# Performance work log

Hardware: AMD Instinct MI355X
Metric: run time of the kernel (lower is better)

The kernel has to match this reference:

```python
import jax, jax.numpy as jnp
import numpy as np

TIME_SEG_LEN = 5
PRED_STEPS = 1
B, N, D = 4, 4096, 4
F1, F2 = 32, 64  # cnn filters; F2 must equal GCSConv/Dense width 64


def _conv1d_time(x, Wc1, bc1, Wc2, bc2):
    # x: [B, N, T, D] -> per-node temporal CNN collapsing T=5 -> 1 -> [B, N, F2]
    b, n, t, d = x.shape
    xr = x.reshape(b * n, t, d)
    dn = ('NWC', 'WIO', 'NWC')
    h = jax.lax.conv_general_dilated(xr, Wc1, (1,), 'VALID', dimension_numbers=dn) + bc1
    h = jax.nn.relu(h)
    h = jax.lax.conv_general_dilated(h, Wc2, (1,), 'VALID', dimension_numbers=dn) + bc2
    return h.reshape(b, n, -1)  # [B, N, F2]


def setup_inputs() -> dict:
    key = jax.random.key(0)
    ks = jax.random.split(key, 12)
    time_segs = jax.random.normal(ks[0], (B, TIME_SEG_LEN, N, D), dtype=jnp.float32)
    edges = jax.random.randint(ks[1], (N, N), 0, 2, dtype=jnp.int32)
    s = lambda *sh: 1.0 / np.sqrt(sh[-2] if len(sh) > 1 else sh[0])
    return {
        'time_segs': time_segs,
        'edges': edges,
        'Wc1': jax.random.normal(ks[2], (3, D, F1), dtype=jnp.float32) * 0.3,
        'bc1': jnp.zeros((F1,), jnp.float32),
        'Wc2': jax.random.normal(ks[3], (3, F1, F2), dtype=jnp.float32) * 0.1,
        'bc2': jnp.zeros((F2,), jnp.float32),
        'Wg1': jax.random.normal(ks[4], (F2, 64), dtype=jnp.float32) * 0.125,
        'bg': jnp.zeros((64,), jnp.float32),
        'Wd': jax.random.normal(ks[5], (F2 + 64, 64), dtype=jnp.float32) * 0.09,
        'bd': jnp.zeros((64,), jnp.float32),
        'Wo': jax.random.normal(ks[6], (64, D), dtype=jnp.float32) * 0.125,
        'bo': jnp.zeros((D,), jnp.float32),
    }


def reference(time_segs, edges, Wc1, bc1, Wc2, bc2, Wg1, bg, Wd, bd, Wo, bo):
    A = edges.astype(jnp.float32)
    n = A.shape[0]
    deg = jnp.sum(A, axis=-1, keepdims=True)              # row degree
    A_norm = A / jnp.where(deg > 0, deg, 1.0)             # D^-1 A (symmetric=False)
    A_nd = A_norm * (1.0 - jnp.eye(n, dtype=A.dtype))     # self-edge masking of X row j == zeroing diag
    col_deg = jnp.sum(A, axis=0)                          # e = np.sum(edges, axis=0)
    alive = (col_deg != 0).astype(time_segs.dtype)[None, :, None]  # zero-degree nodes -> zeros branch

    ext = jnp.transpose(time_segs, (0, 2, 1, 3))          # [B, N, T, D]
    for i in range(PRED_STEPS):
        seg = ext[:, :, i:, :]                            # [B, N, 5, D]
        cond = _conv1d_time(seg, Wc1, bc1, Wc2, bc2)      # [B, N, F2]
        # Vectorized per-node masked GCSConv: row j of tanh(A X_j W1 + X_j W2 + b)
        # with X_j = X zeroed at node j. Skip term vanishes at row j.
        agg = jnp.einsum('jk,bkf->bjf', A_nd, cond)       # [B, N, F2]
        G = jnp.tanh(agg @ Wg1 + bg) * alive              # [B, N, 64]
        h = jax.nn.relu(jnp.concatenate([cond, G], axis=-1) @ Wd + bd)
        nxt = seg[:, :, -1, :] + jnp.tanh(h @ Wo + bo)    # residual update [B, N, D]
        ext = jnp.concatenate([ext, nxt[:, :, None, :]], axis=2)
    out = jnp.transpose(ext, (0, 2, 1, 3))                # [B, T+P, N, D]
    return out[:, TIME_SEG_LEN:, :, :]                    # [B, pred_steps, N, D]
```

## Files before the change

### kernel.cpp

```cpp
#include <hip/hip_runtime.h>
#include <math.h>

typedef unsigned short ushort_t;
typedef unsigned int uint_t;
typedef unsigned long long u64_t;
typedef __attribute__((ext_vector_type(8))) __bf16 bf16x8;
typedef __attribute__((ext_vector_type(4))) float f32x4;

#define NN 4096
#define TT 5
#define F1 32
#define F2 64

__device__ __forceinline__ ushort_t f2bf(float x) {
    union { float f; uint_t u; } v; v.f = x;
    uint_t r = (v.u + 0x7FFFu + ((v.u >> 16) & 1u)) >> 16;
    return (ushort_t)r;
}
__device__ __forceinline__ uint_t pk2(float a, float b) {
    return (uint_t)f2bf(a) | ((uint_t)f2bf(b) << 16);
}
__device__ __forceinline__ float tanh_fast(float x) {
    const float xc = fminf(fmaxf(x, -10.f), 10.f);
    const float e = __expf(2.f * xc);
    return (e - 1.f) * __builtin_amdgcn_rcpf(e + 1.f);
}

__global__ __launch_bounds__(256) void k0_prep(
    const float* __restrict__ Wc2, const float* __restrict__ Wg1, const float* __restrict__ Wd,
    ushort_t* __restrict__ Wc2T_ws, ushort_t* __restrict__ WgT_ws, ushort_t* __restrict__ WdT_ws,
    int* __restrict__ degI, uint_t* __restrict__ colbits)
{
    const int blk = blockIdx.x, t = threadIdx.x;
    if (blk == 0) {
        const uint4 z = make_uint4(0, 0, 0, 0);
        for (int i = t; i < 1024; i += 256) ((uint4*)degI)[i] = z;
        if (t < 32) ((uint4*)colbits)[t] = z;
    } else if (blk == 1) {
        for (int i = t; i < 6144; i += 256) {
            const int e = i >> 6, f = i & 63;
            Wc2T_ws[f * 96 + e] = f2bf(Wc2[i]);
        }
    } else if (blk == 2) {
        for (int i = t; i < 4096; i += 256) {
            const int in = i >> 6, o = i & 63;
            WgT_ws[o * 64 + in] = f2bf(Wg1[i]);
        }
    } else {
        for (int i = t; i < 8192; i += 256) {
            const int in = i >> 6, o = i & 63;
            WdT_ws[o * 128 + in] = f2bf(Wd[i]);
        }
    }
}

#define H1S 104
#define CBS 80
__global__ __launch_bounds__(256) void k1_cond(
    const float* __restrict__ ts, const float* __restrict__ Wc1, const float* __restrict__ bc1,
    const ushort_t* __restrict__ Wc2T_ws, const float* __restrict__ bc2,
    ushort_t* __restrict__ condT, ushort_t* __restrict__ condB)
{
    const int b = blockIdx.y;
    const int j0 = blockIdx.x * 64;
    const int t = threadIdx.x;

    __shared__ float sWc1[384];
    __shared__ float sbc1[F1];
    __shared__ float sbc2[F2];
    __shared__ ushort_t sWc2T[64 * H1S];
    __shared__ ushort_t h1B[64 * H1S];
    __shared__ ushort_t scb[64 * CBS];

    for (int i = t; i < 384; i += 256) sWc1[i] = Wc1[i];
    if (t < F1) sbc1[t] = bc1[t];
    if (t < F2) sbc2[t] = bc2[t];
    for (int i = t; i < 768; i += 256) {
        const int f = i / 12, c = i - f * 12;
        *(uint4*)&sWc2T[f * H1S + c * 8] = *(const uint4*)(Wc2T_ws + f * 96 + c * 8);
    }
    __syncthreads();

    {
        const int n = t & 63, f10 = (t >> 6) * 8;
        const int j = j0 + n;
        float4 x[5];
        #pragma unroll
        for (int tt = 0; tt < 5; ++tt)
            x[tt] = *(const float4*)(ts + ((((size_t)b * TT + tt) << 12) + j) * 4);
        #pragma unroll
        for (int tt0 = 0; tt0 < 3; ++tt0) {
            #pragma unroll
            for (int ff = 0; ff < 8; ++ff) {
                const int f1 = f10 + ff;
                float a = sbc1[f1];
                #pragma unroll
                for (int dt = 0; dt < 3; ++dt) {
                    const float4 xx = x[tt0 + dt];
                    a += xx.x * sWc1[(dt * 4 + 0) * F1 + f1];
                    a += xx.y * sWc1[(dt * 4 + 1) * F1 + f1];
                    a += xx.z * sWc1[(dt * 4 + 2) * F1 + f1];
                    a += xx.w * sWc1[(dt * 4 + 3) * F1 + f1];
                }
                h1B[n * H1S + tt0 * 32 + f1] = f2bf(fmaxf(a, 0.f));
            }
        }
    }
    __syncthreads();

    {
        const int w = t >> 6, l = t & 63;
        const int m0 = w * 16, kseg = (l >> 4) * 8;
        f32x4 acc[4] = {};
        #pragma unroll
        for (int ks = 0; ks < 3; ++ks) {
            const bf16x8 av = *(const bf16x8*)&h1B[(m0 + (l & 15)) * H1S + ks * 32 + kseg];
            #pragma unroll
            for (int ct = 0; ct < 4; ++ct) {
                const bf16x8 bv = *(const bf16x8*)&sWc2T[(ct * 16 + (l & 15)) * H1S + ks * 32 + kseg];
                acc[ct] = __builtin_amdgcn_mfma_f32_16x16x32_bf16(av, bv, acc[ct], 0, 0, 0);
            }
        }
        #pragma unroll
        for (int ct = 0; ct < 4; ++ct)
            #pragma unroll
            for (int i = 0; i < 4; ++i) {
                const int row = m0 + (l >> 4) * 4 + i;
                const int col = ct * 16 + (l & 15);
                scb[col * CBS + row] = f2bf(acc[ct][i] + sbc2[col]);
            }
    }
    __syncthreads();
    {
        const int f2 = t >> 2, seg = t & 3;
        ushort_t* dst = condT + (((size_t)b * 64 + f2) << 12) + j0 + seg * 16;
        *(uint4*)dst = *(const uint4*)&scb[f2 * CBS + seg * 16];
        *(uint4*)(dst + 8) = *(const uint4*)&scb[f2 * CBS + seg * 16 + 8];
    }
    {
        const int r = t >> 2, q = t & 3;
        uint_t u[8];
        #pragma unroll
        for (int k = 0; k < 8; ++k)
            u[k] = (uint_t)scb[(q * 16 + 2 * k) * CBS + r] |
                   ((uint_t)scb[(q * 16 + 2 * k + 1) * CBS + r] << 16);
        ushort_t* dstB = condB + ((((size_t)b << 12) + j0 + r) << 6) + q * 16;
        *(uint4*)dstB = make_uint4(u[0], u[1], u[2], u[3]);
        *(uint4*)(dstB + 8) = make_uint4(u[4], u[5], u[6], u[7]);
    }
}

__global__ __launch_bounds__(1024, 8) void k3_gemm(
    const int* __restrict__ edges, const ushort_t* __restrict__ condT,
    float* __restrict__ agg0, float* __restrict__ agg1,
    float* __restrict__ agg2, float* __restrict__ agg3,
    int* __restrict__ degI, uint_t* __restrict__ colbits,
    unsigned char* __restrict__ diagB)
{
    const int t = threadIdx.x;
    const int stripe = blockIdx.x >> 2, ks4 = blockIdx.x & 3;
    const int j0 = stripe * 32, kb = ks4 * 1024;

    __shared__ __align__(16) ushort_t abuf[8][4096];
    __shared__ uint_t colsh[32];
    __shared__ int sdeg[32];

    const int rl = t & 15, wq = (t >> 4) & 31, rh = t >> 9;
    const int row = j0 + rh * 16 + rl;
    const int* ep = edges + (size_t)row * NN + kb + wq * 32;
    int4 v[8];
    #pragma unroll
    for (int c = 0; c < 8; ++c) v[c] = *(const int4*)(ep + c * 4);
    if (t < 32) { colsh[t] = 0; sdeg[t] = 0; }
    uint_t bw = 0;
    #pragma unroll
    for (int c = 0; c < 8; ++c) {
        const uint_t nib = (v[c].x != 0 ? 1u : 0u) | (v[c].y != 0 ? 2u : 0u) |
                           (v[c].z != 0 ? 4u : 0u) | (v[c].w != 0 ? 8u : 0u);
        bw |= nib << (c * 4);
    }
    {
        ushort_t* dst = &abuf[wq >> 2][rh * 2048 + (wq & 3) * 512];
        #pragma unroll
        for (int o = 0; o < 4; ++o) {
            const uint_t oct = bw >> (o * 8);
            uint4 wv;
            wv.x = ((oct & 1u)   ? 0x3F80u : 0u) | ((oct & 2u)   ? 0x3F800000u : 0u);
            wv.y = ((oct & 4u)   ? 0x3F80u : 0u) | ((oct & 8u)   ? 0x3F800000u : 0u);
            wv.z = ((oct & 16u)  ? 0x3F80u : 0u) | ((oct & 32u)  ? 0x3F800000u : 0u);
            wv.w = ((oct & 64u)  ? 0x3F80u : 0u) | ((oct & 128u) ? 0x3F800000u : 0u);
            *(uint4*)(dst + o * 128 + ((rl * 8) ^ (o << 4))) = wv;
        }
    }
    if (((row - kb) >> 5) == wq)
        diagB[row] = (unsigned char)((bw >> ((row - kb) & 31)) & 1u);
    int s = __popc(bw);
    s += __shfl_down(s, 16);
    s += __shfl_down(s, 32);
    __syncthreads();
    if ((t & 63) < 16) atomicAdd(&sdeg[rh * 16 + rl], s);
    atomicOr(&colsh[wq], bw);

    const int w = t >> 6, l = t & 63;
    const int aoff = (l * 8) ^ ((l >> 4) << 4);
    const ushort_t* bp = condT + (size_t)(w * 16 + (l & 15)) * NN + kb + (l >> 4) * 8;

    f32x4 acc0 = {0.f, 0.f, 0.f, 0.f};
    f32x4 acc1 = {0.f, 0.f, 0.f, 0.f};

    #pragma unroll
    for (int ch = 0; ch < 8; ++ch) {
        const ushort_t* ab = &abuf[ch][0];
        const ushort_t* bpi = bp + ch * 128;
        #pragma unroll
        for (int ks = 0; ks < 4; ++ks) {
            const bf16x8 bfv = *(const bf16x8*)(bpi + ks * 32);
            const bf16x8 a0 = *(const bf16x8*)(ab + ks * 512 + aoff);
            const bf16x8 a1 = *(const bf16x8*)(ab + 2048 + ks * 512 + aoff);
            acc0 = __builtin_amdgcn_mfma_f32_16x16x32_bf16(a0, bfv, acc0, 0, 0, 0);
            acc1 = __builtin_amdgcn_mfma_f32_16x16x32_bf16(a1, bfv, acc1, 0, 0, 0);
        }
    }

    {
        float* aggS = (ks4 == 0) ? agg0 : (ks4 == 1) ? agg1 : (ks4 == 2) ? agg2 : agg3;
        const int col = w * 16 + (l & 15);
        float* dst = aggS + ((size_t)(col >> 6) * NN << 6) + (col & 63);
        #pragma unroll
        for (int i = 0; i < 4; ++i) {
            const int ja = j0 + (l >> 4) * 4 + i;
            dst[(size_t)ja << 6] = acc0[i];
            dst[(size_t)(ja + 16) << 6] = acc1[i];
        }
    }
    __syncthreads();
    if (t < 32) {
        atomicOr(&colbits[(kb >> 5) + t], colsh[t]);
        atomicAdd(&degI[j0 + t], sdeg[t]);
    }
}

#define WGS 88
#define WDS 136
#define HS  69
__global__ __launch_bounds__(256) void k4_mlp(
    const float* __restrict__ ts, const ushort_t* __restrict__ condB,
    const float* __restrict__ agg0, const float* __restrict__ agg1,
    const float* __restrict__ agg2, const float* __restrict__ agg3,
    const int* __restrict__ degI, const uint_t* __restrict__ colbits,
    const unsigned char* __restrict__ diagB,
    const ushort_t* __restrict__ WgT_ws, const float* __restrict__ bg,
    const ushort_t* __restrict__ WdT_ws, const float* __restrict__ bd,
    const float* __restrict__ Wo, const float* __restrict__ bo,
    float* __restrict__ out)
{
    const int b = blockIdx.y;
    const int j0 = blockIdx.x * 64;
    const int t = threadIdx.x;

    __shared__ ushort_t sWg1T[64 * WGS];
    __shared__ ushort_t sWdT[64 * WDS];
    __shared__ ushort_t aggB[64 * WGS];
    __shared__ ushort_t catB[64 * WDS];
    __shared__ float sH[64 * HS];
    __shared__ float sWo[256];
    __shared__ float sbg[64], sbd[64], sbo[4], sAlive[64];

    for (int i = t; i < 512; i += 256)
        *(uint4*)&sWg1T[(i >> 3) * WGS + (i & 7) * 8] = ((const uint4*)WgT_ws)[i];
    for (int i = t; i < 1024; i += 256)
        *(uint4*)&sWdT[(i >> 4) * WDS + (i & 15) * 8] = ((const uint4*)WdT_ws)[i];
    if (t < 256) sWo[t] = Wo[t];
    if (t < 64) { sbg[t] = bg[t]; sbd[t] = bd[t]; }
    if (t < 4) sbo[t] = bo[t];
    if (t < 64) {
        const int j = j0 + t;
        sAlive[t] = (float)((colbits[j >> 5] >> (j & 31)) & 1u);
    }
    {
        const int r = t >> 2, fs = t & 3;
        const int j = j0 + r;
        const float dv = (float)degI[j];
        const float inv = 1.f / (dv > 0.f ? dv : 1.f);
        const float dgf = (float)diagB[j];
        const size_t base = (((size_t)b << 12) + j) << 6;
        const uint4 c0 = *(const uint4*)(condB + base + fs * 16);
        const uint4 c1 = *(const uint4*)(condB + base + fs * 16 + 8);
        *(uint4*)&catB[r * WDS + fs * 16] = c0;
        *(uint4*)&catB[r * WDS + fs * 16 + 8] = c1;
        #pragma unroll
        for (int q = 0; q < 4; ++q) {
            uint_t wlo, whi;
            if (q == 0)      { wlo = c0.x; whi = c0.y; }
            else if (q == 1) { wlo = c0.z; whi = c0.w; }
            else if (q == 2) { wlo = c1.x; whi = c1.y; }
            else             { wlo = c1.z; whi = c1.w; }
            const int f = fs * 16 + q * 4;
            const float4 a0 = *(const float4*)(agg0 + base + f);
            const float4 a1 = *(const float4*)(agg1 + base + f);
            const float4 a2 = *(const float4*)(agg2 + base + f);
            const float4 a3 = *(const float4*)(agg3 + base + f);
            const float cv0 = __uint_as_float(wlo << 16);
            const float cv1 = __uint_as_float(wlo & 0xFFFF0000u);
            const float cv2 = __uint_as_float(whi << 16);
            const float cv3 = __uint_as_float(whi & 0xFFFF0000u);
            const float n0 = (a0.x + a1.x + a2.x + a3.x - dgf * cv0) * inv;
            const float n1 = (a0.y + a1.y + a2.y + a3.y - dgf * cv1) * inv;
            const float n2 = (a0.z + a1.z + a2.z + a3.z - dgf * cv2) * inv;
            const float n3 = (a0.w + a1.w + a2.w + a3.w - dgf * cv3) * inv;
            *(uint2*)&aggB[r * WGS + f] = make_uint2(pk2(n0, n1), pk2(n2, n3));
        }
    }
    __syncthreads();

    const int w = t >> 6, l = t & 63;
    const int m0 = w * 16, kseg = (l >> 4) * 8;

    {
        f32x4 acc[4] = {};
        #pragma unroll
        for (int ks = 0; ks < 2; ++ks) {
            const bf16x8 av = *(const bf16x8*)&aggB[(m0 + (l & 15)) * WGS + ks * 32 + kseg];
            #pragma unroll
            for (int ct = 0; ct < 4; ++ct) {
                const bf16x8 bv = *(const bf16x8*)&sWg1T[(ct * 16 + (l & 15)) * WGS + ks * 32 + kseg];
                acc[ct] = __builtin_amdgcn_mfma_f32_16x16x32_bf16(av, bv, acc[ct], 0, 0, 0);
            }
        }
        #pragma unroll
        for (int ct = 0; ct < 4; ++ct)
            #pragma unroll
            for (int i = 0; i < 4; ++i) {
                const int row = m0 + (l >> 4) * 4 + i;
                const int col = ct * 16 + (l & 15);
                const float g = tanh_fast(acc[ct][i] + sbg[col]) * sAlive[row];
                catB[row * WDS + 64 + col] = f2bf(g);
            }
    }
    __syncthreads();
    {
        f32x4 acc[4] = {};
        #pragma unroll
        for (int ks = 0; ks < 4; ++ks) {
            const bf16x8 av = *(const bf16x8*)&catB[(m0 + (l & 15)) * WDS + ks * 32 + kseg];
            #pragma unroll
            for (int ct = 0; ct < 4; ++ct) {
                const bf16x8 bv = *(const bf16x8*)&sWdT[(ct * 16 + (l & 15)) * WDS + ks * 32 + kseg];
                acc[ct] = __builtin_amdgcn_mfma_f32_16x16x32_bf16(av, bv, acc[ct], 0, 0, 0);
            }
        }
        #pragma unroll
        for (int ct = 0; ct < 4; ++ct)
            #pragma unroll
            for (int i = 0; i < 4; ++i) {
                const int row = m0 + (l >> 4) * 4 + i;
                const int col = ct * 16 + (l & 15);
                sH[row * HS + col] = fmaxf(acc[ct][i] + sbd[col], 0.f);
            }
    }
    __syncthreads();
    {
        const int r = t >> 2, d = t & 3;
        const int j = j0 + r;
        float s = sbo[d];
        #pragma unroll 8
        for (int f = 0; f < 64; ++f) s += sH[r * HS + f] * sWo[f * 4 + d];
        const float segl = ts[((((size_t)b * TT + 4) << 12) + j) * 4 + d];
        out[((((size_t)b << 12) + j) << 2) + d] = segl + tanh_fast(s);
    }
}

extern "C" void kernel_launch(void* const* d_in, const int* in_sizes, int n_in,
                              void* d_out, int out_size, void* d_ws, size_t ws_size,
                              hipStream_t stream)
{
    (void)in_sizes; (void)n_in; (void)out_size; (void)ws_size;
    const float* ts    = (const float*)d_in[0];
    const int*   edges = (const int*)d_in[1];
    const float* Wc1   = (const float*)d_in[2];
    const float* bc1   = (const float*)d_in[3];
    const float* Wc2   = (const float*)d_in[4];
    const float* bc2   = (const float*)d_in[5];
    const float* Wg1   = (const float*)d_in[6];
    const float* bg    = (const float*)d_in[7];
    const float* Wd    = (const float*)d_in[8];
    const float* bd    = (const float*)d_in[9];
    const float* Wo    = (const float*)d_in[10];
    const float* bo    = (const float*)d_in[11];
    float* out = (float*)d_out;

    char* ws = (char*)d_ws;
    ushort_t* condT   = (ushort_t*)(ws);
    ushort_t* condB   = (ushort_t*)(ws + (size_t)(2 << 20));
    float*    agg0    = (float*)(ws + (size_t)(4 << 20));
    float*    agg1    = (float*)(ws + (size_t)(8 << 20));
    float*    agg2    = (float*)(ws + (size_t)(12 << 20));
    float*    agg3    = (float*)(ws + (size_t)(16 << 20));
    int*      degI    = (int*)(ws + (size_t)(20 << 20));
    uint_t*   colbits = (uint_t*)(ws + (size_t)(20 << 20) + 16384);
    unsigned char* diagB = (unsigned char*)(ws + (size_t)(20 << 20) + 16896);
    ushort_t* WgT_ws  = (ushort_t*)(ws + (size_t)(20 << 20) + 20992);
    ushort_t* WdT_ws  = (ushort_t*)(ws + (size_t)(20 << 20) + 29184);
    ushort_t* Wc2T_ws = (ushort_t*)(ws + (size_t)(20 << 20) + 45568);

    k0_prep<<<4, 256, 0, stream>>>(Wc2, Wg1, Wd, Wc2T_ws, WgT_ws, WdT_ws, degI, colbits);
    k1_cond<<<dim3(64, 4), 256, 0, stream>>>(ts, Wc1, bc1, Wc2T_ws, bc2, condT, condB);
    k3_gemm<<<512, 1024, 0, stream>>>(edges, condT, agg0, agg1, agg2, agg3,
                                      degI, colbits, diagB);
    k4_mlp<<<dim3(64, 4), 256, 0, stream>>>(ts, condB, agg0, agg1, agg2, agg3,
                                            degI, colbits, diagB,
                                            WgT_ws, bg, WdT_ws, bd, Wo, bo, out);
}
```

Before: 174.2 us.

## Split edge bit-packing and degree computation into a separate kernel before GEMM

Adds a k2_bits kernel that reads the int32 adjacency matrix once, packs it into a bitmask in workspace, and computes row degrees, column-alive bits and diagonal flags without atomics on degI. The GEMM kernel then reads compact packed bits instead of 64 MB of int32 edges and drops its shared-memory reductions and global atomics. This adds a kernel launch and a bits write plus read round-trip, but both kernels keep the same total edge traffic while the GEMM becomes lighter.

```diff
diff --git a/kernel.cpp b/kernel.cpp
--- a/kernel.cpp
+++ b/kernel.cpp
@@ -29,13 +29,11 @@
 __global__ __launch_bounds__(256) void k0_prep(
     const float* __restrict__ Wc2, const float* __restrict__ Wg1, const float* __restrict__ Wd,
     ushort_t* __restrict__ Wc2T_ws, ushort_t* __restrict__ WgT_ws, ushort_t* __restrict__ WdT_ws,
-    int* __restrict__ degI, uint_t* __restrict__ colbits)
+    uint_t* __restrict__ colbits)
 {
     const int blk = blockIdx.x, t = threadIdx.x;
     if (blk == 0) {
-        const uint4 z = make_uint4(0, 0, 0, 0);
-        for (int i = t; i < 1024; i += 256) ((uint4*)degI)[i] = z;
-        if (t < 32) ((uint4*)colbits)[t] = z;
+        if (t < 32) ((uint4*)colbits)[t] = make_uint4(0, 0, 0, 0);
     } else if (blk == 1) {
         for (int i = t; i < 6144; i += 256) {
             const int e = i >> 6, f = i & 63;
@@ -52,6 +50,52 @@
             WdT_ws[o * 128 + in] = f2bf(Wd[i]);
         }
     }
+}
+
+__global__ __launch_bounds__(1024, 4) void k2_bits(
+    const int4* __restrict__ edges4, uint_t* __restrict__ bits,
+    int* __restrict__ degI, uint_t* __restrict__ colbits, unsigned char* __restrict__ diagB)
+{
+    const int t = threadIdx.x;
+    const int bid = blockIdx.x;
+    __shared__ int sdeg[16][8];
+
+    int4 v[8];
+    #pragma unroll
+    for (int s = 0; s < 8; ++s)
+        v[s] = edges4[(size_t)s * 524288 + (size_t)bid * 1024 + (size_t)t];
+
+    const int w = t >> 6, l = t & 63;
+    const int nsh = (t & 7) * 4;
+    uint_t creg = 0;
+    #pragma unroll
+    for (int s = 0; s < 8; ++s) {
+        const int row = s * 512 + bid;
+        const uint_t nib = (v[s].x != 0 ? 1u : 0u) | (v[s].y != 0 ? 2u : 0u) |
+                           (v[s].z != 0 ? 4u : 0u) | (v[s].w != 0 ? 8u : 0u);
+        uint_t part = nib << nsh;
+        part |= __shfl_xor(part, 1);
+        part |= __shfl_xor(part, 2);
+        part |= __shfl_xor(part, 4);
+        if ((t & 7) == 0) {
+            bits[(size_t)row * 128 + (size_t)(t >> 3)] = part;
+            creg |= part;
+            if ((t >> 3) == (row >> 5))
+                diagB[row] = (unsigned char)((part >> (row & 31)) & 1u);
+        }
+        int p = __popc(nib);
+        #pragma unroll
+        for (int off = 32; off >= 1; off >>= 1) p += __shfl_down(p, off);
+        if (l == 0) sdeg[w][s] = p;
+    }
+    __syncthreads();
+    if (t < 8) {
+        int s2 = 0;
+        #pragma unroll
+        for (int w2 = 0; w2 < 16; ++w2) s2 += sdeg[w2][t];
+        degI[t * 512 + bid] = s2;
+    }
+    if ((t & 7) == 0) atomicOr(&colbits[t >> 3], creg);
 }
 
 #define H1S 104
@@ -151,34 +195,18 @@
 }
 
 __global__ __launch_bounds__(1024, 8) void k3_gemm(
-    const int* __restrict__ edges, const ushort_t* __restrict__ condT,
+    const uint_t* __restrict__ bits, const ushort_t* __restrict__ condT,
     float* __restrict__ agg0, float* __restrict__ agg1,
-    float* __restrict__ agg2, float* __restrict__ agg3,
-    int* __restrict__ degI, uint_t* __restrict__ colbits,
-    unsigned char* __restrict__ diagB)
+    float* __restrict__ agg2, float* __restrict__ agg3)
 {
     const int t = threadIdx.x;
     const int stripe = blockIdx.x >> 2, ks4 = blockIdx.x & 3;
     const int j0 = stripe * 32, kb = ks4 * 1024;
 
     __shared__ __align__(16) ushort_t abuf[8][4096];
-    __shared__ uint_t colsh[32];
-    __shared__ int sdeg[32];
 
     const int rl = t & 15, wq = (t >> 4) & 31, rh = t >> 9;
-    const int row = j0 + rh * 16 + rl;
-    const int* ep = edges + (size_t)row * NN + kb + wq * 32;
-    int4 v[8];
-    #pragma unroll
-    for (int c = 0; c < 8; ++c) v[c] = *(const int4*)(ep + c * 4);
-    if (t < 32) { colsh[t] = 0; sdeg[t] = 0; }
-    uint_t bw = 0;
-    #pragma unroll
-    for (int c = 0; c < 8; ++c) {
-        const uint_t nib = (v[c].x != 0 ? 1u : 0u) | (v[c].y != 0 ? 2u : 0u) |
-                           (v[c].z != 0 ? 4u : 0u) | (v[c].w != 0 ? 8u : 0u);
-        bw |= nib << (c * 4);
-    }
+    const uint_t bw = bits[(size_t)(j0 + rh * 16 + rl) * 128 + (size_t)(kb >> 5) + (size_t)wq];
     {
         ushort_t* dst = &abuf[wq >> 2][rh * 2048 + (wq & 3) * 512];
         #pragma unroll
@@ -192,14 +220,7 @@
             *(uint4*)(dst + o * 128 + ((rl * 8) ^ (o << 4))) = wv;
         }
     }
-    if (((row - kb) >> 5) == wq)
-        diagB[row] = (unsigned char)((bw >> ((row - kb) & 31)) & 1u);
-    int s = __popc(bw);
-    s += __shfl_down(s, 16);
-    s += __shfl_down(s, 32);
-    __syncthreads();
-    if ((t & 63) < 16) atomicAdd(&sdeg[rh * 16 + rl], s);
-    atomicOr(&colsh[wq], bw);
+    __syncthreads();
 
     const int w = t >> 6, l = t & 63;
     const int aoff = (l * 8) ^ ((l >> 4) << 4);
@@ -232,11 +253,6 @@
             dst[(size_t)ja << 6] = acc0[i];
             dst[(size_t)(ja + 16) << 6] = acc1[i];
         }
-    }
-    __syncthreads();
-    if (t < 32) {
-        atomicOr(&colbits[(kb >> 5) + t], colsh[t]);
-        atomicAdd(&degI[j0 + t], sdeg[t]);
     }
 }
 
@@ -402,11 +418,12 @@
     ushort_t* WgT_ws  = (ushort_t*)(ws + (size_t)(20 << 20) + 20992);
     ushort_t* WdT_ws  = (ushort_t*)(ws + (size_t)(20 << 20) + 29184);
     ushort_t* Wc2T_ws = (ushort_t*)(ws + (size_t)(20 << 20) + 45568);
-
-    k0_prep<<<4, 256, 0, stream>>>(Wc2, Wg1, Wd, Wc2T_ws, WgT_ws, WdT_ws, degI, colbits);
+    uint_t*   bits    = (uint_t*)(ws + (size_t)(21 << 20));
+
+    k0_prep<<<4, 256, 0, stream>>>(Wc2, Wg1, Wd, Wc2T_ws, WgT_ws, WdT_ws, colbits);
+    k2_bits<<<512, 1024, 0, stream>>>((const int4*)edges, bits, degI, colbits, diagB);
     k1_cond<<<dim3(64, 4), 256, 0, stream>>>(ts, Wc1, bc1, Wc2T_ws, bc2, condT, condB);
-    k3_gemm<<<512, 1024, 0, stream>>>(edges, condT, agg0, agg1, agg2, agg3,
-                                      degI, colbits, diagB);
+    k3_gemm<<<512, 1024, 0, stream>>>(bits, condT, agg0, agg1, agg2, agg3);
     k4_mlp<<<dim3(64, 4), 256, 0, stream>>>(ts, condB, agg0, agg1, agg2, agg3,
                                             degI, colbits, diagB,
                                             WgT_ws, bg, WdT_ws, bd, Wo, bo, out);
```

New measurement: 189.7 us. 8.9% more time.

## Split edge bit-packing into separate kernel and fold weight prep into consumers

Applied to the files above, without the earlier changes.

A new k2_bits kernel reads the int32 adjacency once, packs it into a 2 MB bitmask, and computes row degrees with plain stores plus column-alive bits and diagonal flags. The GEMM kernel then reads the compact bits instead of the 64 MB edge matrix and drops its shared-memory atomics and tail reductions. The weight-transpose prep kernel is removed: k1 and k4 now convert and transpose weights from fp32 directly into shared memory, and a memset replaces the colbits zeroing. This adds a launch and a bitmask round trip through memory, and repeats the weight conversion in every block.

```diff
diff --git a/kernel.cpp b/kernel.cpp
--- a/kernel.cpp
+++ b/kernel.cpp
@@ -26,39 +26,53 @@
     return (e - 1.f) * __builtin_amdgcn_rcpf(e + 1.f);
 }
 
-__global__ __launch_bounds__(256) void k0_prep(
-    const float* __restrict__ Wc2, const float* __restrict__ Wg1, const float* __restrict__ Wd,
-    ushort_t* __restrict__ Wc2T_ws, ushort_t* __restrict__ WgT_ws, ushort_t* __restrict__ WdT_ws,
-    int* __restrict__ degI, uint_t* __restrict__ colbits)
+__global__ __launch_bounds__(1024, 8) void k2_bits(
+    const int4* __restrict__ edges4, uint_t* __restrict__ bits,
+    int* __restrict__ degI, uint_t* __restrict__ colbits, unsigned char* __restrict__ diagB)
 {
-    const int blk = blockIdx.x, t = threadIdx.x;
-    if (blk == 0) {
-        const uint4 z = make_uint4(0, 0, 0, 0);
-        for (int i = t; i < 1024; i += 256) ((uint4*)degI)[i] = z;
-        if (t < 32) ((uint4*)colbits)[t] = z;
-    } else if (blk == 1) {
-        for (int i = t; i < 6144; i += 256) {
-            const int e = i >> 6, f = i & 63;
-            Wc2T_ws[f * 96 + e] = f2bf(Wc2[i]);
-        }
-    } else if (blk == 2) {
-        for (int i = t; i < 4096; i += 256) {
-            const int in = i >> 6, o = i & 63;
-            WgT_ws[o * 64 + in] = f2bf(Wg1[i]);
-        }
-    } else {
-        for (int i = t; i < 8192; i += 256) {
-            const int in = i >> 6, o = i & 63;
-            WdT_ws[o * 128 + in] = f2bf(Wd[i]);
-        }
-    }
+    const int t = threadIdx.x;
+    const int bid = blockIdx.x;
+    const uint_t W = (uint_t)bid * 1024u + (uint_t)t;
+    __shared__ uint_t colsh[128];
+    __shared__ int sdeg[16];
+
+    const int4* ep = edges4 + (size_t)W * 8;
+    int4 v[8];
+    #pragma unroll
+    for (int c = 0; c < 8; ++c) v[c] = ep[c];
+
+    if (t < 128) colsh[t] = 0;
+
+    uint_t bw = 0;
+    #pragma unroll
+    for (int c = 0; c < 8; ++c) {
+        const uint_t nib = (v[c].x != 0 ? 1u : 0u) | (v[c].y != 0 ? 2u : 0u) |
+                           (v[c].z != 0 ? 4u : 0u) | (v[c].w != 0 ? 8u : 0u);
+        bw |= nib << (c * 4);
+    }
+    bits[W] = bw;
+
+    const int row = (int)(W >> 7);
+    if ((t & 127) == (row >> 5))
+        diagB[row] = (unsigned char)((bw >> (row & 31)) & 1u);
+
+    int s = __popc(bw);
+    #pragma unroll
+    for (int off = 32; off >= 1; off >>= 1) s += __shfl_down(s, off);
+    const int w = t >> 6, l = t & 63;
+    if (l == 0) sdeg[w] = s;
+    __syncthreads();
+    atomicOr(&colsh[t & 127], bw);
+    __syncthreads();
+    if (t < 128) atomicOr(&colbits[t], colsh[t]);
+    if (t < 8) degI[bid * 8 + t] = sdeg[2 * t] + sdeg[2 * t + 1];
 }
 
 #define H1S 104
 #define CBS 80
 __global__ __launch_bounds__(256) void k1_cond(
     const float* __restrict__ ts, const float* __restrict__ Wc1, const float* __restrict__ bc1,
-    const ushort_t* __restrict__ Wc2T_ws, const float* __restrict__ bc2,
+    const float* __restrict__ Wc2, const float* __restrict__ bc2,
     ushort_t* __restrict__ condT, ushort_t* __restrict__ condB)
 {
     const int b = blockIdx.y;
@@ -75,9 +89,9 @@
     for (int i = t; i < 384; i += 256) sWc1[i] = Wc1[i];
     if (t < F1) sbc1[t] = bc1[t];
     if (t < F2) sbc2[t] = bc2[t];
-    for (int i = t; i < 768; i += 256) {
-        const int f = i / 12, c = i - f * 12;
-        *(uint4*)&sWc2T[f * H1S + c * 8] = *(const uint4*)(Wc2T_ws + f * 96 + c * 8);
+    for (int i = t; i < 96 * 64; i += 256) {
+        const int e = i >> 6, f = i & 63;
+        sWc2T[f * H1S + e] = f2bf(Wc2[i]);
     }
     __syncthreads();
 
@@ -151,34 +165,18 @@
 }
 
 __global__ __launch_bounds__(1024, 8) void k3_gemm(
-    const int* __restrict__ edges, const ushort_t* __restrict__ condT,
+    const uint_t* __restrict__ bits, const ushort_t* __restrict__ condT,
     float* __restrict__ agg0, float* __restrict__ agg1,
-    float* __restrict__ agg2, float* __restrict__ agg3,
-    int* __restrict__ degI, uint_t* __restrict__ colbits,
-    unsigned char* __restrict__ diagB)
+    float* __restrict__ agg2, float* __restrict__ agg3)
 {
     const int t = threadIdx.x;
     const int stripe = blockIdx.x >> 2, ks4 = blockIdx.x & 3;
     const int j0 = stripe * 32, kb = ks4 * 1024;
 
     __shared__ __align__(16) ushort_t abuf[8][4096];
-    __shared__ uint_t colsh[32];
-    __shared__ int sdeg[32];
 
     const int rl = t & 15, wq = (t >> 4) & 31, rh = t >> 9;
-    const int row = j0 + rh * 16 + rl;
-    const int* ep = edges + (size_t)row * NN + kb + wq * 32;
-    int4 v[8];
-    #pragma unroll
-    for (int c = 0; c < 8; ++c) v[c] = *(const int4*)(ep + c * 4);
-    if (t < 32) { colsh[t] = 0; sdeg[t] = 0; }
-    uint_t bw = 0;
-    #pragma unroll
-    for (int c = 0; c < 8; ++c) {
-        const uint_t nib = (v[c].x != 0 ? 1u : 0u) | (v[c].y != 0 ? 2u : 0u) |
-                           (v[c].z != 0 ? 4u : 0u) | (v[c].w != 0 ? 8u : 0u);
-        bw |= nib << (c * 4);
-    }
+    const uint_t bw = bits[(size_t)(j0 + rh * 16 + rl) * 128 + (size_t)(kb >> 5) + (size_t)wq];
     {
         ushort_t* dst = &abuf[wq >> 2][rh * 2048 + (wq & 3) * 512];
         #pragma unroll
@@ -192,14 +190,7 @@
             *(uint4*)(dst + o * 128 + ((rl * 8) ^ (o << 4))) = wv;
         }
     }
-    if (((row - kb) >> 5) == wq)
-        diagB[row] = (unsigned char)((bw >> ((row - kb) & 31)) & 1u);
-    int s = __popc(bw);
-    s += __shfl_down(s, 16);
-    s += __shfl_down(s, 32);
-    __syncthreads();
-    if ((t & 63) < 16) atomicAdd(&sdeg[rh * 16 + rl], s);
-    atomicOr(&colsh[wq], bw);
+    __syncthreads();
 
     const int w = t >> 6, l = t & 63;
     const int aoff = (l * 8) ^ ((l >> 4) << 4);
@@ -232,11 +223,6 @@
             dst[(size_t)ja << 6] = acc0[i];
             dst[(size_t)(ja + 16) << 6] = acc1[i];
         }
-    }
-    __syncthreads();
-    if (t < 32) {
-        atomicOr(&colbits[(kb >> 5) + t], colsh[t]);
-        atomicAdd(&degI[j0 + t], sdeg[t]);
     }
 }
 
@@ -249,8 +235,8 @@
     const float* __restrict__ agg2, const float* __restrict__ agg3,
     const int* __restrict__ degI, const uint_t* __restrict__ colbits,
     const unsigned char* __restrict__ diagB,
-    const ushort_t* __restrict__ WgT_ws, const float* __restrict__ bg,
-    const ushort_t* __restrict__ WdT_ws, const float* __restrict__ bd,
+    const float* __restrict__ Wg1, const float* __restrict__ bg,
+    const float* __restrict__ Wd, const float* __restrict__ bd,
     const float* __restrict__ Wo, const float* __restrict__ bo,
     float* __restrict__ out)
 {
@@ -266,10 +252,14 @@
     __shared__ float sWo[256];
     __shared__ float sbg[64], sbd[64], sbo[4], sAlive[64];
 
-    for (int i = t; i < 512; i += 256)
-        *(uint4*)&sWg1T[(i >> 3) * WGS + (i & 7) * 8] = ((const uint4*)WgT_ws)[i];
-    for (int i = t; i < 1024; i += 256)
-        *(uint4*)&sWdT[(i >> 4) * WDS + (i & 15) * 8] = ((const uint4*)WdT_ws)[i];
+    for (int i = t; i < 4096; i += 256) {
+        const int in = i >> 6, o = i & 63;
+        sWg1T[o * WGS + in] = f2bf(Wg1[i]);
+    }
+    for (int i = t; i < 8192; i += 256) {
+        const int in = i >> 6, o = i & 63;
+        sWdT[o * WDS + in] = f2bf(Wd[i]);
+    }
     if (t < 256) sWo[t] = Wo[t];
     if (t < 64) { sbg[t] = bg[t]; sbd[t] = bd[t]; }
     if (t < 4) sbo[t] = bo[t];
@@ -399,15 +389,13 @@
     int*      degI    = (int*)(ws + (size_t)(20 << 20));
     uint_t*   colbits = (uint_t*)(ws + (size_t)(20 << 20) + 16384);
     unsigned char* diagB = (unsigned char*)(ws + (size_t)(20 << 20) + 16896);
-    ushort_t* WgT_ws  = (ushort_t*)(ws + (size_t)(20 << 20) + 20992);
-    ushort_t* WdT_ws  = (ushort_t*)(ws + (size_t)(20 << 20) + 29184);
-    ushort_t* Wc2T_ws = (ushort_t*)(ws + (size_t)(20 << 20) + 45568);
-
-    k0_prep<<<4, 256, 0, stream>>>(Wc2, Wg1, Wd, Wc2T_ws, WgT_ws, WdT_ws, degI, colbits);
-    k1_cond<<<dim3(64, 4), 256, 0, stream>>>(ts, Wc1, bc1, Wc2T_ws, bc2, condT, condB);
-    k3_gemm<<<512, 1024, 0, stream>>>(edges, condT, agg0, agg1, agg2, agg3,
-                                      degI, colbits, diagB);
+    uint_t*   bits    = (uint_t*)(ws + (size_t)(21 << 20));
+
+    hipMemsetAsync(colbits, 0, 512, stream);
+    k2_bits<<<512, 1024, 0, stream>>>((const int4*)edges, bits, degI, colbits, diagB);
+    k1_cond<<<dim3(64, 4), 256, 0, stream>>>(ts, Wc1, bc1, Wc2, bc2, condT, condB);
+    k3_gemm<<<512, 1024, 0, stream>>>(bits, condT, agg0, agg1, agg2, agg3);
     k4_mlp<<<dim3(64, 4), 256, 0, stream>>>(ts, condB, agg0, agg1, agg2, agg3,
                                             degI, colbits, diagB,
-                                            WgT_ws, bg, WdT_ws, bd, Wo, bo, out);
-}
+                                            Wg1, bg, Wd, bd, Wo, bo, out);
+}
```

New measurement: 172.8 us. About the same (-0.8%).
